# Optimization experiments

Measured on AMD Instinct MI355X. Metric: run time of the kernel, lower is better.

## Reference

```python
import jax, jax.numpy as jnp
import numpy as np
from jax import lax

B, C, H, W = 32, 1, 224, 224
OUT, K, STRIDE, PAD = 64, 5, 1, 2
D = C * K * K

def _make_weight(key):
    # torch kaiming_uniform_(a=0, fan_in=D, gain=sqrt(2)): bound = sqrt(6/fan_in)
    bound = np.sqrt(6.0 / D)
    w = jax.random.uniform(key, (OUT, D), jnp.float32, -bound, bound)
    w = w.at[0].set(-1.0)
    w = w.at[1].set(1.0)
    return w

def setup_inputs() -> dict:
    key = jax.random.key(0)
    kx, kw = jax.random.split(key)
    x = jax.random.normal(kx, (B, C, H, W), jnp.float32)
    weight = _make_weight(kw)
    return {"x": x, "weight": weight}

def reference(x, weight):
    # im2col: [B, C*K*K, H', W']  (channel-major patch ordering matches torch unfold for C=1)
    patches = lax.conv_general_dilated_patches(
        x, (K, K), (STRIDE, STRIDE), [(PAD, PAD), (PAD, PAD)])
    b, d, hp, wp = patches.shape
    win = patches.reshape(b, d, hp * wp).transpose(0, 2, 1)  # [B, L, D]
    x2 = jnp.sum(win * win, axis=-1, keepdims=True)          # [B, L, 1]
    w2 = jnp.sum(weight * weight, axis=-1)                   # [O]
    xw = jnp.einsum('bld,od->blo', win, weight)              # [B, L, O]
    d2 = jnp.maximum(x2 + w2[None, None, :] - 2.0 * xw, 0.0)
    dist = jnp.sqrt(d2)                                      # [B, L, O]
    return dist.transpose(0, 2, 1).reshape(b, OUT, hp, wp)
```

## Files before the change

### kernel.cpp

```cpp
#include <hip/hip_runtime.h>

#define BB    32
#define HH    224
#define WW    224
#define OUTC  64
#define KK    5
#define PADP  2
#define LL    (HH * WW)

__global__ __launch_bounds__(256) void gray_conv_kernel(
    const float* __restrict__ x,
    const float* __restrict__ wgt,
    float* __restrict__ out)
{
    __shared__ float sw[OUTC][28];
    __shared__ float sw2[OUTC];

    const int tid = threadIdx.x;

    for (int i = tid; i < OUTC * 25; i += 256) {
        sw[i / 25][i % 25] = wgt[i];
    }
    __syncthreads();
    if (tid < OUTC) {
        float s = 0.f;
        #pragma unroll
        for (int d = 0; d < 25; ++d) { float v = sw[tid][d]; s = fmaf(v, v, s); }
        sw2[tid] = s;
    }
    __syncthreads();

    const int pos = blockIdx.x * 256 + tid;
    const int b   = pos / LL;
    const int rem = pos - b * LL;
    const int h   = rem / WW;
    const int w   = rem - h * WW;

    const float* xb = x + (size_t)b * LL;

    float p[25];
    float x2 = 0.f;
    #pragma unroll
    for (int ky = 0; ky < KK; ++ky) {
        const int  yy  = h + ky - PADP;
        const int  yc  = min(max(yy, 0), HH - 1);
        const bool oky = (unsigned)yy < (unsigned)HH;
        #pragma unroll
        for (int kx = 0; kx < KK; ++kx) {
            const int  xx = w + kx - PADP;
            const int  xc = min(max(xx, 0), WW - 1);
            const bool ok = oky && ((unsigned)xx < (unsigned)WW);
            float v = xb[yc * WW + xc];
            v = ok ? v : 0.f;
            p[ky * KK + kx] = v;
            x2 = fmaf(v, v, x2);
        }
    }

    float* ob = out + (size_t)b * OUTC * LL + rem;
    #pragma unroll 4
    for (int o = 0; o < OUTC; ++o) {
        float dot = 0.f;
        #pragma unroll
        for (int d = 0; d < 25; ++d) dot = fmaf(p[d], sw[o][d], dot);
        float d2 = fmaf(-2.f, dot, x2 + sw2[o]);
        d2 = fmaxf(d2, 0.f);
        ob[(size_t)o * LL] = sqrtf(d2);
    }
}

extern "C" void kernel_launch(void* const* d_in, const int* in_sizes, int n_in,
                              void* d_out, int out_size, void* d_ws, size_t ws_size,
                              hipStream_t stream) {
    const float* x   = (const float*)d_in[0];
    const float* wgt = (const float*)d_in[1];
    float* out       = (float*)d_out;

    const int total  = BB * LL;
    const int blocks = total / 256;
    gray_conv_kernel<<<dim3(blocks), dim3(256), 0, stream>>>(x, wgt, out);
}
```

Baseline: 472.4 us.

## Compute four adjacent pixels per thread with shared window and float4 stores

Each thread now handles four horizontally adjacent output positions. It loads a 5x8 input window once and reuses each channel's weights across the four dot products. Results are written with a single float4 store per channel, and the fast hardware sqrt replaces sqrtf. This is meant to cut shared-memory weight reads and redundant input loads per output, at the cost of more registers per thread and a quarter as many threads.

```diff
diff --git a/kernel.cpp b/kernel.cpp
--- a/kernel.cpp
+++ b/kernel.cpp
@@ -7,6 +7,7 @@
 #define KK    5
 #define PADP  2
 #define LL    (HH * WW)
+#define GPB   (LL / 4)
 
 __global__ __launch_bounds__(256) void gray_conv_kernel(
     const float* __restrict__ x,
@@ -30,42 +31,81 @@
     }
     __syncthreads();
 
-    const int pos = blockIdx.x * 256 + tid;
-    const int b   = pos / LL;
-    const int rem = pos - b * LL;
+    const int g   = blockIdx.x * 256 + tid;
+    const int b   = g / GPB;
+    const int gr  = g - b * GPB;
+    const int rem = gr * 4;
     const int h   = rem / WW;
-    const int w   = rem - h * WW;
+    const int w0  = rem - h * WW;
 
     const float* xb = x + (size_t)b * LL;
 
-    float p[25];
-    float x2 = 0.f;
+    int  xc[8];
+    bool okc[8];
     #pragma unroll
-    for (int ky = 0; ky < KK; ++ky) {
-        const int  yy  = h + ky - PADP;
+    for (int c = 0; c < 8; ++c) {
+        const int xx = w0 + c - PADP;
+        xc[c]  = min(max(xx, 0), WW - 1);
+        okc[c] = (unsigned)xx < (unsigned)WW;
+    }
+
+    float p[5][8];
+    #pragma unroll
+    for (int r = 0; r < KK; ++r) {
+        const int  yy  = h + r - PADP;
         const int  yc  = min(max(yy, 0), HH - 1);
-        const bool oky = (unsigned)yy < (unsigned)HH;
+        const bool okr = (unsigned)yy < (unsigned)HH;
+        const float* xrow = xb + yc * WW;
         #pragma unroll
-        for (int kx = 0; kx < KK; ++kx) {
-            const int  xx = w + kx - PADP;
-            const int  xc = min(max(xx, 0), WW - 1);
-            const bool ok = oky && ((unsigned)xx < (unsigned)WW);
-            float v = xb[yc * WW + xc];
-            v = ok ? v : 0.f;
-            p[ky * KK + kx] = v;
-            x2 = fmaf(v, v, x2);
+        for (int c = 0; c < 8; ++c) {
+            float v = xrow[xc[c]];
+            p[r][c] = (okr && okc[c]) ? v : 0.f;
         }
     }
 
+    float x2[4];
+    #pragma unroll
+    for (int j = 0; j < 4; ++j) {
+        float s = 0.f;
+        #pragma unroll
+        for (int r = 0; r < KK; ++r)
+            #pragma unroll
+            for (int k = 0; k < KK; ++k) {
+                const float v = p[r][j + k];
+                s = fmaf(v, v, s);
+            }
+        x2[j] = s;
+    }
+
     float* ob = out + (size_t)b * OUTC * LL + rem;
-    #pragma unroll 4
+
     for (int o = 0; o < OUTC; ++o) {
-        float dot = 0.f;
+        float wv[25];
         #pragma unroll
-        for (int d = 0; d < 25; ++d) dot = fmaf(p[d], sw[o][d], dot);
-        float d2 = fmaf(-2.f, dot, x2 + sw2[o]);
-        d2 = fmaxf(d2, 0.f);
-        ob[(size_t)o * LL] = sqrtf(d2);
+        for (int d = 0; d < 25; ++d) wv[d] = sw[o][d];
+        const float w2 = sw2[o];
+
+        float dot[4];
+        #pragma unroll
+        for (int j = 0; j < 4; ++j) {
+            float s = 0.f;
+            #pragma unroll
+            for (int r = 0; r < KK; ++r)
+                #pragma unroll
+                for (int k = 0; k < KK; ++k)
+                    s = fmaf(p[r][j + k], wv[r * KK + k], s);
+            dot[j] = s;
+        }
+
+        float r4[4];
+        #pragma unroll
+        for (int j = 0; j < 4; ++j) {
+            float d2 = fmaf(-2.f, dot[j], x2[j] + w2);
+            d2 = fmaxf(d2, 0.f);
+            r4[j] = __builtin_amdgcn_sqrtf(d2);
+        }
+        *reinterpret_cast<float4*>(ob + (size_t)o * LL) =
+            make_float4(r4[0], r4[1], r4[2], r4[3]);
     }
 }
 
@@ -76,7 +116,7 @@
     const float* wgt = (const float*)d_in[1];
     float* out       = (float*)d_out;
 
-    const int total  = BB * LL;
-    const int blocks = total / 256;
+    const int groups = BB * GPB;
+    const int blocks = groups / 256;
     gray_conv_kernel<<<dim3(blocks), dim3(256), 0, stream>>>(x, wgt, out);
 }
```

Measured after the change: 437.8 us. 1.08x faster.
